# Kernel tuning notes

Measured on AMD Instinct MI355X. Metric: run time of the kernel, lower is better.

## Reference

```python
import jax, jax.numpy as jnp
import numpy as np
from jax import lax

EPS = 1e-5  # BatchNorm / LayerNorm eps
B, DIM, H, W = 32, 256, 64, 64
S = 64            # state_dim
D_INNER = 256     # ssd_expand * dim
HIDDEN = 1024     # mlp_ratio * dim


def _bn(x, g, b, m, v):
    # BatchNorm2d, inference mode with given running stats. x: (B,C,H,W)
    inv = lax.rsqrt(v + EPS)
    return (x - m[None, :, None, None]) * (g * inv)[None, :, None, None] + b[None, :, None, None]


def _dwconv3x3(x, w):
    # depthwise 3x3 conv, stride 1, SAME padding. w: (C,1,3,3)
    return lax.conv_general_dilated(
        x, w, window_strides=(1, 1), padding='SAME',
        feature_group_count=x.shape[1],
        dimension_numbers=('NCHW', 'OIHW', 'NCHW'))


def setup_inputs() -> dict:
    key = jax.random.key(0)
    ks = jax.random.split(key, 32)
    n = lambda i, shp, s=0.02: jax.random.normal(ks[i], shp, jnp.float32) * s
    u = lambda i, shp: jax.random.uniform(ks[i], shp, jnp.float32)
    return {
        'x': jax.random.normal(ks[0], (B, DIM, H, W), jnp.float32),
        # dwconv1 (Conv2dNorm depthwise)
        'dw1_w': n(1, (DIM, 1, 3, 3)), 'dw1_g': 1.0 + n(2, (DIM,)), 'dw1_b': n(3, (DIM,)),
        'dw1_m': n(4, (DIM,)), 'dw1_v': u(5, (DIM,)) + 0.5,
        # LayerNorm1d
        'ln_w': 1.0 + n(6, (DIM,)), 'ln_b': n(7, (DIM,)),
        # mixer (HSMSSD)
        'bcdt_w': n(8, (3 * S, DIM)),
        'dwm_w': n(9, (3 * S, 1, 3, 3)),
        'A_param': 1.0 + 15.0 * u(10, (S,)),
        'hz_w': n(11, (2 * D_INNER, DIM)),
        'out_w': n(12, (DIM, D_INNER)),
        'D_param': jnp.ones((1,), jnp.float32),
        # dwconv2
        'dw2_w': n(13, (DIM, 1, 3, 3)), 'dw2_g': 1.0 + n(14, (DIM,)), 'dw2_b': n(15, (DIM,)),
        'dw2_m': n(16, (DIM,)), 'dw2_v': u(17, (DIM,)) + 0.5,
        # FFN
        'fc1_w': n(18, (HIDDEN, DIM)), 'fc1_g': 1.0 + n(19, (HIDDEN,)), 'fc1_b': n(20, (HIDDEN,)),
        'fc1_m': n(21, (HIDDEN,)), 'fc1_v': u(22, (HIDDEN,)) + 0.5,
        'fc2_w': n(23, (DIM, HIDDEN)), 'fc2_g': 1.0 + n(24, (DIM,)), 'fc2_b': n(25, (DIM,)),
        'fc2_m': n(26, (DIM,)), 'fc2_v': u(27, (DIM,)) + 0.5,
        # alpha-gated residual blends
        'alpha': 1e-4 * jnp.ones((4, DIM), jnp.float32) + n(28, (4, DIM), 0.01),
    }


def reference(x, dw1_w, dw1_g, dw1_b, dw1_m, dw1_v, ln_w, ln_b,
              bcdt_w, dwm_w, A_param, hz_w, out_w, D_param,
              dw2_w, dw2_g, dw2_b, dw2_m, dw2_v,
              fc1_w, fc1_g, fc1_b, fc1_m, fc1_v,
              fc2_w, fc2_g, fc2_b, fc2_m, fc2_v, alpha):
    b, dim, h_, w_ = x.shape
    L = h_ * w_
    a = jax.nn.sigmoid(alpha)[:, :, None, None]  # (4, dim, 1, 1)

    # alpha-blended depthwise conv 1
    x = (1.0 - a[0]) * x + a[0] * _bn(_dwconv3x3(x, dw1_w), dw1_g, dw1_b, dw1_m, dw1_v)
    x_prev = x

    # LayerNorm1d over channel dim on (B, C, L)
    xf = x.reshape(b, dim, L)
    mean = xf.mean(axis=1, keepdims=True)
    var = ((xf - mean) ** 2).mean(axis=1, keepdims=True)
    xn = (xf - mean) * lax.rsqrt(var + EPS) * ln_w[None, :, None] + ln_b[None, :, None]

    # HSMSSD mixer
    bc_dt = jnp.einsum('bcl,oc->bol', xn, bcdt_w).reshape(b, 3 * S, h_, w_)
    bc_dt = _dwconv3x3(bc_dt, dwm_w).reshape(b, 3 * S, L)
    Bm, Cm, dt = jnp.split(bc_dt, 3, axis=1)          # each (B, S, L)
    Am = jax.nn.softmax(dt + A_param[None, :, None], axis=-1)
    AB = Am * Bm                                      # (B, S, L)
    h = jnp.einsum('bcl,bsl->bcs', xn, AB)            # (B, dim, S)
    hz = jnp.einsum('bcs,oc->bos', h, hz_w)           # (B, 2*d_inner, S)
    hh, z = jnp.split(hz, 2, axis=1)
    hg = hh * jax.nn.silu(z) + hh * D_param[0]
    hout = jnp.einsum('bcs,oc->bos', hg, out_w)       # (B, dim, S)
    y = jnp.einsum('bcs,bsl->bcl', hout, Cm).reshape(b, dim, h_, w_)

    x = (1.0 - a[1]) * x_prev + a[1] * y
    x = (1.0 - a[2]) * x + a[2] * _bn(_dwconv3x3(x, dw2_w), dw2_g, dw2_b, dw2_m, dw2_v)

    # FFN: 1x1 conv + BN + ReLU + 1x1 conv + BN
    t = _bn(jnp.einsum('bchw,oc->bohw', x, fc1_w), fc1_g, fc1_b, fc1_m, fc1_v)
    t = jax.nn.relu(t)
    t = _bn(jnp.einsum('bchw,oc->bohw', t, fc2_w), fc2_g, fc2_b, fc2_m, fc2_v)
    x = (1.0 - a[3]) * x + a[3] * t
    return (x, hout)
```

## Files before the change

### kernel.cpp

```cpp
#include <hip/hip_runtime.h>
#include <hip/hip_bf16.h>

typedef __hip_bfloat16 bf16;
typedef __attribute__((ext_vector_type(8))) short bf16x8;
typedef __attribute__((ext_vector_type(4))) float f32x4;

__device__ __forceinline__ float LD(const float* p){ return *p; }
__device__ __forceinline__ float LD(const bf16* p){ return __bfloat162float(*p); }
__device__ __forceinline__ void ST(float* p, float v){ *p = v; }
__device__ __forceinline__ void ST(bf16* p, float v){ *p = __float2bfloat16(v); }
__device__ __forceinline__ float sigm(float v){ return 1.f/(1.f + expf(-v)); }
__device__ __forceinline__ ushort f2b(float f){
    unsigned u = __float_as_uint(f);
    return (ushort)((u + 0x7fffu + ((u>>16)&1u)) >> 16);
}

#define NEPS 1e-5f

__global__ __launch_bounds__(256) void dwconv_bn_blend(
        const float* __restrict__ xin, float* __restrict__ xout,
        const float* __restrict__ w, const float* __restrict__ gg, const float* __restrict__ bb,
        const float* __restrict__ mm, const float* __restrict__ vv,
        const float* __restrict__ alpha, int arow)
{
    __shared__ float tile[66*66];
    int blk = blockIdx.x;
    int ch = blk & 255;
    const float* xp = xin + (size_t)blk*4096;
    float* op = xout + (size_t)blk*4096;
    int tid = threadIdx.x;
    for (int i = tid; i < 66*66; i += 256) {
        int r = i/66, c = i%66;
        int gr = r-1, gc = c-1;
        float val = 0.f;
        if (gr >= 0 && gr < 64 && gc >= 0 && gc < 64) val = xp[gr*64+gc];
        tile[i] = val;
    }
    __syncthreads();
    float wv[9];
    #pragma unroll
    for (int k=0;k<9;k++) wv[k] = w[ch*9+k];
    float sc = gg[ch] * rsqrtf(vv[ch] + NEPS);
    float mv = mm[ch], bv = bb[ch];
    float av = sigm(alpha[arow*256+ch]);
    for (int p = tid; p < 4096; p += 256) {
        int r = p>>6, c = p&63;
        float a = 0.f;
        #pragma unroll
        for (int dr=0;dr<3;dr++)
            #pragma unroll
            for (int dc=0;dc<3;dc++)
                a += wv[dr*3+dc]*tile[(r+dr)*66 + (c+dc)];
        float bn = (a - mv)*sc + bv;
        float xv = tile[(r+1)*66 + (c+1)];
        op[p] = (1.f-av)*xv + av*bn;
    }
}

__global__ __launch_bounds__(256) void ln_stats(const float* __restrict__ x1,
        float* __restrict__ meanp, float* __restrict__ invp)
{
    int blk = blockIdx.x;
    int b = blk >> 4;
    int l = ((blk & 15) << 8) + threadIdx.x;
    const float* xp = x1 + (size_t)b*256*4096 + l;
    float mean = 0.f, m2 = 0.f;
    for (int c=0;c<256;c++){ float v = xp[(size_t)c*4096]; mean += v; m2 += v*v; }
    mean *= (1.f/256.f); m2 *= (1.f/256.f);
    meanp[b*4096 + l] = mean;
    invp[b*4096 + l] = rsqrtf(m2 - mean*mean + NEPS);
}

__global__ __launch_bounds__(256) void prep_k(
        const float* __restrict__ f1w, const float* __restrict__ f2w,
        const float* __restrict__ bcdtw,
        const float* __restrict__ g1, const float* __restrict__ b1,
        const float* __restrict__ m1, const float* __restrict__ v1,
        const float* __restrict__ g2, const float* __restrict__ b2,
        const float* __restrict__ m2, const float* __restrict__ v2,
        ushort* __restrict__ w1bf, ushort* __restrict__ w2bf,
        ushort* __restrict__ wbc,
        float* __restrict__ sc1, float* __restrict__ sb1,
        float* __restrict__ sc2, float* __restrict__ sb2)
{
    int i = blockIdx.x*256 + threadIdx.x;
    if (i < 262144) {
        w1bf[i] = f2b(f1w[i]);
        w2bf[i] = f2b(f2w[i]);
    }
    if (i < 49152) wbc[i] = f2b(bcdtw[i]);
    if (i < 1024) { float s = g1[i]*rsqrtf(v1[i]+NEPS); sc1[i]=s; sb1[i]=b1[i]-m1[i]*s; }
    if (i < 256)  { float s = g2[i]*rsqrtf(v2[i]+NEPS); sc2[i]=s; sb2[i]=b2[i]-m2[i]*s; }
}

__global__ __launch_bounds__(256) void bcdt_mfma(
        const float* __restrict__ x1,
        const float* __restrict__ meanp, const float* __restrict__ invp,
        const float* __restrict__ lnw, const float* __restrict__ lnb,
        const ushort* __restrict__ wbc,
        bf16* __restrict__ bc, ushort* __restrict__ xn_bf, int b0)
{
    __shared__ __align__(16) ushort Xs[64*256];
    int blk = blockIdx.x;
    int lb = blk >> 6;
    int b  = b0 + lb;
    int l0 = (blk & 63) << 6;
    int tid = threadIdx.x, lane = tid & 63, w = tid >> 6;
    const float* xp = x1 + (size_t)b*256*4096 + l0;
    float mval = meanp[b*4096 + l0 + lane];
    float ival = invp [b*4096 + l0 + lane];
    ushort* xnp = xn_bf + (size_t)lb*256*4096 + l0;

    for (int cc = w*8; cc < 256; cc += 32) {
        ushort u[8];
        #pragma unroll
        for (int j=0;j<8;j++){
            float v = xp[(size_t)(cc+j)*4096 + lane];
            float xn = (v - mval)*ival*lnw[cc+j] + lnb[cc+j];
            u[j] = f2b(xn);
            xnp[(size_t)(cc+j)*4096 + lane] = u[j];
        }
        uint4 pk;
        pk.x = (uint)u[0] | ((uint)u[1]<<16);
        pk.y = (uint)u[2] | ((uint)u[3]<<16);
        pk.z = (uint)u[4] | ((uint)u[5]<<16);
        pk.w = (uint)u[6] | ((uint)u[7]<<16);
        int g = (cc>>3) ^ (lane&7);
        *(uint4*)&Xs[lane*256 + g*8] = pk;
    }
    __syncthreads();

    f32x4 zero4 = {0.f,0.f,0.f,0.f};
    f32x4 acc[3][4];
    #pragma unroll
    for (int m=0;m<3;m++)
        #pragma unroll
        for (int f=0;f<4;f++) acc[m][f] = zero4;

    int hbase = w*48;
    #pragma unroll
    for (int ks=0; ks<8; ks++){
        bf16x8 afr[3];
        #pragma unroll
        for (int m=0;m<3;m++)
            afr[m] = *(const bf16x8*)&wbc[(size_t)(hbase + m*16 + (lane&15))*256
                                          + ks*32 + (lane>>4)*8];
        #pragma unroll
        for (int f=0;f<4;f++){
            int px = f*16 + (lane&15);
            int g = (ks*4 + (lane>>4)) ^ (px&7);
            bf16x8 bfr = *(const bf16x8*)&Xs[px*256 + g*8];
            #pragma unroll
            for (int m=0;m<3;m++)
                acc[m][f] = __builtin_amdgcn_mfma_f32_16x16x32_bf16(afr[m], bfr, acc[m][f], 0,0,0);
        }
    }
    bf16* op = bc + (size_t)lb*192*4096 + l0;
    #pragma unroll
    for (int m=0;m<3;m++)
        #pragma unroll
        for (int r=0;r<4;r++){
            int o = hbase + m*16 + (lane>>4)*4 + r;
            #pragma unroll
            for (int f=0;f<4;f++){
                int px = f*16 + (lane&15);
                op[(size_t)o*4096 + px] = __float2bfloat16(acc[m][f][r]);
            }
        }
}

__global__ __launch_bounds__(256) void dwconv_plain(bf16* __restrict__ data, const float* __restrict__ w)
{
    __shared__ float tile[66*66];
    int blk = blockIdx.x;
    int ch = blk % 192;
    bf16* xp = data + (size_t)blk*4096;
    int tid = threadIdx.x;
    for (int i = tid; i < 66*66; i += 256) {
        int r = i/66, c = i%66;
        int gr = r-1, gc = c-1;
        float val = 0.f;
        if (gr >= 0 && gr < 64 && gc >= 0 && gc < 64) val = LD(&xp[gr*64+gc]);
        tile[i] = val;
    }
    __syncthreads();
    float wv[9];
    #pragma unroll
    for (int k=0;k<9;k++) wv[k] = w[ch*9+k];
    for (int p = tid; p < 4096; p += 256) {
        int r = p>>6, c = p&63;
        float a = 0.f;
        #pragma unroll
        for (int dr=0;dr<3;dr++)
            #pragma unroll
            for (int dc=0;dc<3;dc++)
                a += wv[dr*3+dc]*tile[(r+dr)*66 + (c+dc)];
        ST(&xp[p], a);
    }
}

__global__ __launch_bounds__(256) void softmax_ab(bf16* __restrict__ bc, const float* __restrict__ A)
{
    __shared__ float red[8];
    int blk = blockIdx.x;
    int lb = blk >> 6;
    int s = blk & 63;
    bf16* dtp = bc + ((size_t)lb*192 + 128 + s)*4096;
    bf16* bmp = bc + ((size_t)lb*192 + s)*4096;
    int tid = threadIdx.x;
    float Av = A[s];
    float vals[16];
    float mx = -1e30f;
    #pragma unroll
    for (int i=0;i<16;i++){ vals[i] = LD(&dtp[i*256+tid]) + Av; mx = fmaxf(mx, vals[i]); }
    #pragma unroll
    for (int o=32;o>0;o>>=1) mx = fmaxf(mx, __shfl_down(mx, o));
    int lane = tid & 63, wid = tid >> 6;
    if (lane == 0) red[wid] = mx;
    __syncthreads();
    if (tid == 0) red[4] = fmaxf(fmaxf(red[0],red[1]), fmaxf(red[2],red[3]));
    __syncthreads();
    mx = red[4];
    float sum = 0.f;
    #pragma unroll
    for (int i=0;i<16;i++){ vals[i] = expf(vals[i]-mx); sum += vals[i]; }
    #pragma unroll
    for (int o=32;o>0;o>>=1) sum += __shfl_down(sum, o);
    if (lane == 0) red[wid] = sum;
    __syncthreads();
    if (tid == 0) red[5] = red[0]+red[1]+red[2]+red[3];
    __syncthreads();
    float inv = 1.f/red[5];
    #pragma unroll
    for (int i=0;i<16;i++){
        float ab = vals[i]*inv*LD(&bmp[i*256+tid]);
        ST(&bmp[i*256+tid], ab);
    }
}

__global__ __launch_bounds__(256) void h_mfma(
        const ushort* __restrict__ xn_bf, const bf16* __restrict__ bc,
        float* __restrict__ h_part)
{
    int blk = blockIdx.x;
    int lb = blk >> 3;
    int kz = blk & 7;
    int kbase = kz*512;
    int tid = threadIdx.x, lane = tid & 63, w = tid >> 6;
    const ushort* ap = xn_bf + (size_t)lb*256*4096;
    const ushort* bp = (const ushort*)bc + (size_t)lb*192*4096;
    f32x4 zero4 = {0.f,0.f,0.f,0.f};
    f32x4 acc[4][4];
    #pragma unroll
    for (int m=0;m<4;m++)
        #pragma unroll
        for (int n=0;n<4;n++) acc[m][n] = zero4;

    for (int ks=0; ks<16; ks++){
        int koff = kbase + ks*32 + (lane>>4)*8;
        bf16x8 afr[4], bfr[4];
        #pragma unroll
        for (int m=0;m<4;m++)
            afr[m] = *(const bf16x8*)&ap[(size_t)(w*64 + m*16 + (lane&15))*4096 + koff];
        #pragma unroll
        for (int n=0;n<4;n++)
            bfr[n] = *(const bf16x8*)&bp[(size_t)(n*16 + (lane&15))*4096 + koff];
        #pragma unroll
        for (int m=0;m<4;m++)
            #pragma unroll
            for (int n=0;n<4;n++)
                acc[m][n] = __builtin_amdgcn_mfma_f32_16x16x32_bf16(afr[m], bfr[n], acc[m][n], 0,0,0);
    }
    float* hp = h_part + ((size_t)lb*8 + kz)*16384;
    #pragma unroll
    for (int m=0;m<4;m++)
        #pragma unroll
        for (int n=0;n<4;n++)
            #pragma unroll
            for (int r=0;r<4;r++){
                int c = w*64 + m*16 + (lane>>4)*4 + r;
                int s = n*16 + (lane&15);
                hp[c*64 + s] = acc[m][n][r];
            }
}

__global__ __launch_bounds__(256) void hz_gemm(const float* __restrict__ h_part,
        const float* __restrict__ w, float* __restrict__ hz)
{
    __shared__ float ht[256][64];
    int blk = blockIdx.x; int lb = blk>>3; int o0 = (blk&7)*64;
    int tid = threadIdx.x;
    const float* hp = h_part + (size_t)lb*8*16384;
    for (int i=tid;i<16384;i+=256){
        float s = 0.f;
        #pragma unroll
        for (int k=0;k<8;k++) s += hp[k*16384 + i];
        ht[i>>6][i&63] = s;
    }
    __syncthreads();
    int lane=tid&63, g=tid>>6;
    for (int i4=0;i4<4;i4++){
        int ol = g*16 + i4*4;
        const float* r0 = w + (size_t)(o0+ol)*256;
        const float *r1=r0+256, *r2=r0+512, *r3=r0+768;
        float d0=0.f,d1=0.f,d2=0.f,d3=0.f;
        #pragma unroll 8
        for (int c4=0;c4<64;c4++){
            float x0=ht[c4*4][lane],x1v=ht[c4*4+1][lane],x2v=ht[c4*4+2][lane],x3v=ht[c4*4+3][lane];
            float4 a0=((const float4*)r0)[c4],a1=((const float4*)r1)[c4];
            float4 a2=((const float4*)r2)[c4],a3=((const float4*)r3)[c4];
            d0 += a0.x*x0+a0.y*x1v+a0.z*x2v+a0.w*x3v;
            d1 += a1.x*x0+a1.y*x1v+a1.z*x2v+a1.w*x3v;
            d2 += a2.x*x0+a2.y*x1v+a2.z*x2v+a2.w*x3v;
            d3 += a3.x*x0+a3.y*x1v+a3.z*x2v+a3.w*x3v;
        }
        size_t base = ((size_t)lb*512 + o0 + ol)*64 + lane;
        hz[base]=d0; hz[base+64]=d1; hz[base+128]=d2; hz[base+192]=d3;
    }
}

__global__ void gate_k(const float* __restrict__ hz, float* __restrict__ hg, const float* __restrict__ Dp)
{
    int i = blockIdx.x*256 + threadIdx.x;
    int lb = i >> 14;
    int r = i & 16383;
    const float* hp = hz + (size_t)lb*32768;
    float hh = hp[r], z = hp[16384 + r];
    float sil = z / (1.f + expf(-z));
    hg[i] = hh * (sil + Dp[0]);
}

__global__ __launch_bounds__(256) void out_gemm(const float* __restrict__ hg, const float* __restrict__ w,
        ushort* __restrict__ hout_bf, float* __restrict__ hout_out, int b0)
{
    __shared__ float ht[256][64];
    int blk = blockIdx.x; int lb = blk>>2; int b = b0 + lb; int o0 = (blk&3)*64;
    int tid = threadIdx.x;
    const float* hp = hg + (size_t)lb*16384;
    for (int i=tid;i<16384;i+=256) ht[i>>6][i&63]=hp[i];
    __syncthreads();
    int lane=tid&63, g=tid>>6;
    for (int i4=0;i4<4;i4++){
        int ol = g*16 + i4*4;
        const float* r0 = w + (size_t)(o0+ol)*256;
        const float *r1=r0+256, *r2=r0+512, *r3=r0+768;
        float d0=0.f,d1=0.f,d2=0.f,d3=0.f;
        #pragma unroll 8
        for (int c4=0;c4<64;c4++){
            float x0=ht[c4*4][lane],x1v=ht[c4*4+1][lane],x2v=ht[c4*4+2][lane],x3v=ht[c4*4+3][lane];
            float4 a0=((const float4*)r0)[c4],a1=((const float4*)r1)[c4];
            float4 a2=((const float4*)r2)[c4],a3=((const float4*)r3)[c4];
            d0 += a0.x*x0+a0.y*x1v+a0.z*x2v+a0.w*x3v;
            d1 += a1.x*x0+a1.y*x1v+a1.z*x2v+a1.w*x3v;
            d2 += a2.x*x0+a2.y*x1v+a2.z*x2v+a2.w*x3v;
            d3 += a3.x*x0+a3.y*x1v+a3.z*x2v+a3.w*x3v;
        }
        size_t lbase = ((size_t)lb*256 + o0 + ol)*64 + lane;
        hout_bf[lbase]=f2b(d0); hout_bf[lbase+64]=f2b(d1);
        hout_bf[lbase+128]=f2b(d2); hout_bf[lbase+192]=f2b(d3);
        size_t gbase = ((size_t)b*256 + o0 + ol)*64 + lane;
        hout_out[gbase]=d0; hout_out[gbase+64]=d1;
        hout_out[gbase+128]=d2; hout_out[gbase+192]=d3;
    }
}

__global__ __launch_bounds__(256) void y_mfma(
        const ushort* __restrict__ hout_bf, const bf16* __restrict__ bc,
        float* __restrict__ x1, const float* __restrict__ alpha, int b0)
{
    __shared__ __align__(16) ushort Cs[64*64];
    int blk = blockIdx.x; int lb = blk>>6; int b = b0 + lb; int l0 = (blk&63)<<6;
    int tid = threadIdx.x, lane = tid&63, w = tid>>6;
    const ushort* cp = (const ushort*)bc + ((size_t)lb*192 + 64)*4096 + l0;
    for (int sc = w*8; sc < 64; sc += 32){
        ushort u[8];
        #pragma unroll
        for (int j=0;j<8;j++) u[j] = cp[(size_t)(sc+j)*4096 + lane];
        uint4 pk;
        pk.x = (uint)u[0] | ((uint)u[1]<<16);
        pk.y = (uint)u[2] | ((uint)u[3]<<16);
        pk.z = (uint)u[4] | ((uint)u[5]<<16);
        pk.w = (uint)u[6] | ((uint)u[7]<<16);
        int g = (sc>>3) ^ (lane&7);
        *(uint4*)&Cs[lane*64 + g*8] = pk;
    }
    __syncthreads();

    f32x4 zero4 = {0.f,0.f,0.f,0.f};
    f32x4 acc[4][4];
    #pragma unroll
    for (int m=0;m<4;m++)
        #pragma unroll
        for (int f=0;f<4;f++) acc[m][f] = zero4;

    const ushort* ap = hout_bf + (size_t)lb*256*64;
    #pragma unroll
    for (int ks=0; ks<2; ks++){
        bf16x8 afr[4];
        #pragma unroll
        for (int m=0;m<4;m++)
            afr[m] = *(const bf16x8*)&ap[(size_t)(w*64 + m*16 + (lane&15))*64
                                          + ks*32 + (lane>>4)*8];
        #pragma unroll
        for (int f=0;f<4;f++){
            int px = f*16 + (lane&15);
            int s8 = ks*32 + (lane>>4)*8;
            int g = (s8>>3) ^ (px&7);
            bf16x8 bfr = *(const bf16x8*)&Cs[px*64 + g*8];
            #pragma unroll
            for (int m=0;m<4;m++)
                acc[m][f] = __builtin_amdgcn_mfma_f32_16x16x32_bf16(afr[m], bfr, acc[m][f], 0,0,0);
        }
    }

    float* xpo = x1 + (size_t)b*256*4096 + l0;
    #pragma unroll
    for (int m=0;m<4;m++)
        #pragma unroll
        for (int r=0;r<4;r++){
            int c = w*64 + m*16 + (lane>>4)*4 + r;
            float av = sigm(alpha[256+c]);
            #pragma unroll
            for (int f=0;f<4;f++){
                int px = f*16 + (lane&15);
                float xv = xpo[(size_t)c*4096 + px];
                xpo[(size_t)c*4096 + px] = (1.f-av)*xv + av*acc[m][f][r];
            }
        }
}

__global__ __launch_bounds__(256) void transpose_k(const float* __restrict__ x1,
        ushort* __restrict__ xT)
{
    __shared__ ushort T[64*258];
    int blk = blockIdx.x;
    int b = blk >> 6, l0 = (blk & 63) << 6;
    int tid = threadIdx.x;
    const float* xp = x1 + (size_t)b*256*4096 + l0;
    for (int i = tid; i < 16384; i += 256){
        int c = i >> 6, l = i & 63;
        T[l*258 + c] = f2b(xp[(size_t)c*4096 + l]);
    }
    __syncthreads();
    int l = tid & 63, cseg = (tid >> 6) << 6;
    ushort* op = xT + ((size_t)b*4096 + l0 + l)*256 + cseg;
    const ushort* tp = &T[l*258 + cseg];
    #pragma unroll
    for (int j=0;j<8;j++){
        uint4 v;
        v.x = (uint)tp[j*8+0] | ((uint)tp[j*8+1]<<16);
        v.y = (uint)tp[j*8+2] | ((uint)tp[j*8+3]<<16);
        v.z = (uint)tp[j*8+4] | ((uint)tp[j*8+5]<<16);
        v.w = (uint)tp[j*8+6] | ((uint)tp[j*8+7]<<16);
        *(uint4*)&op[j*8] = v;
    }
}

__global__ __launch_bounds__(256) void ffn_mfma_t(
        const ushort* __restrict__ xT,
        const float* __restrict__ x,
        const ushort* __restrict__ w1bf,
        const ushort* __restrict__ w2bf,
        const float* __restrict__ sc1, const float* __restrict__ sb1,
        const float* __restrict__ sc2, const float* __restrict__ sb2,
        const float* __restrict__ alpha,
        float* __restrict__ out)
{
    __shared__ __align__(16) ushort Ts[64*128];
    int blk = blockIdx.x;
    int b = blk >> 6, l0 = (blk & 63) << 6;
    int tid = threadIdx.x, lane = tid & 63, w = tid >> 6;
    const ushort* xtp = xT + ((size_t)b*4096 + l0)*256;
    const float* xp = x + (size_t)b*256*4096 + l0;

    f32x4 zero4 = {0.f,0.f,0.f,0.f};
    f32x4 acc2[4][4];
    #pragma unroll
    for (int m=0;m<4;m++)
        #pragma unroll
        for (int f=0;f<4;f++) acc2[m][f] = zero4;

    for (int hc = 0; hc < 1024; hc += 128) {
        int hbase = hc + w*32;
        f32x4 c1[2][4];
        #pragma unroll
        for (int m=0;m<2;m++)
            #pragma unroll
            for (int f=0;f<4;f++) c1[m][f] = zero4;
        for (int ks = 0; ks < 8; ks++) {
            bf16x8 afr[2];
            #pragma unroll
            for (int m=0;m<2;m++)
                afr[m] = *(const bf16x8*)&w1bf[(size_t)(hbase + m*16 + (lane&15))*256
                                               + ks*32 + (lane>>4)*8];
            #pragma unroll
            for (int f=0;f<4;f++){
                bf16x8 bfr = *(const bf16x8*)&xtp[(size_t)(f*16 + (lane&15))*256
                                                  + ks*32 + (lane>>4)*8];
                #pragma unroll
                for (int m=0;m<2;m++)
                    c1[m][f] = __builtin_amdgcn_mfma_f32_16x16x32_bf16(afr[m], bfr, c1[m][f], 0,0,0);
            }
        }
        __syncthreads();
        #pragma unroll
        for (int m=0;m<2;m++){
            int hl0 = w*32 + m*16 + ((lane>>4)<<2);
            int h0 = hc + hl0;
            float s0=sc1[h0], s1=sc1[h0+1], s2=sc1[h0+2], s3=sc1[h0+3];
            float q0=sb1[h0], q1=sb1[h0+1], q2=sb1[h0+2], q3=sb1[h0+3];
            int gbase = hl0>>3;
            #pragma unroll
            for (int f=0;f<4;f++){
                int px = f*16 + (lane&15);
                float t0 = fmaxf(c1[m][f][0]*s0 + q0, 0.f);
                float t1 = fmaxf(c1[m][f][1]*s1 + q1, 0.f);
                float t2 = fmaxf(c1[m][f][2]*s2 + q2, 0.f);
                float t3 = fmaxf(c1[m][f][3]*s3 + q3, 0.f);
                uint2 pk;
                pk.x = (uint)f2b(t0) | ((uint)f2b(t1)<<16);
                pk.y = (uint)f2b(t2) | ((uint)f2b(t3)<<16);
                int g = gbase ^ (px&7);
                *(uint2*)&Ts[px*128 + g*8 + (hl0&7)] = pk;
            }
        }
        __syncthreads();
        int c0 = w*64;
        for (int ks = 0; ks < 4; ks++) {
            bf16x8 afr[4];
            #pragma unroll
            for (int m=0;m<4;m++)
                afr[m] = *(const bf16x8*)&w2bf[(size_t)(c0 + m*16 + (lane&15))*1024
                                               + hc + ks*32 + (lane>>4)*8];
            #pragma unroll
            for (int f=0;f<4;f++){
                int px = f*16 + (lane&15);
                int hl = ks*32 + (lane>>4)*8;
                int g = (hl>>3) ^ (px&7);
                bf16x8 bfr = *(const bf16x8*)&Ts[px*128 + g*8];
                #pragma unroll
                for (int m=0;m<4;m++)
                    acc2[m][f] = __builtin_amdgcn_mfma_f32_16x16x32_bf16(afr[m], bfr, acc2[m][f], 0,0,0);
            }
        }
    }

    float* op = out + (size_t)b*256*4096 + l0;
    int c0 = w*64;
    #pragma unroll
    for (int m=0;m<4;m++){
        #pragma unroll
        for (int r=0;r<4;r++){
            int c = c0 + m*16 + (lane>>4)*4 + r;
            float a = sigm(alpha[768+c]);
            float s2 = sc2[c], bb2 = sb2[c];
            #pragma unroll
            for (int f=0;f<4;f++){
                int px = f*16 + (lane&15);
                float t2 = acc2[m][f][r]*s2 + bb2;
                float xv = xp[(size_t)c*4096 + px];
                op[(size_t)c*4096 + px] = (1.f-a)*xv + a*t2;
            }
        }
    }
}

__global__ __launch_bounds__(256) void ffn_mfma(
        const float* __restrict__ x,
        const ushort* __restrict__ w1bf, const ushort* __restrict__ w2bf,
        const float* __restrict__ sc1, const float* __restrict__ sb1,
        const float* __restrict__ sc2, const float* __restrict__ sb2,
        const float* __restrict__ alpha, float* __restrict__ out)
{
    __shared__ __align__(16) ushort Xs[64*256];
    __shared__ __align__(16) ushort Ts[64*128];
    int blk = blockIdx.x;
    int b = blk >> 6, l0 = (blk & 63) << 6;
    int tid = threadIdx.x, lane = tid & 63, w = tid >> 6;
    const float* xp = x + (size_t)b*256*4096 + l0;

    for (int cc = w*8; cc < 256; cc += 32) {
        float v[8];
        #pragma unroll
        for (int j=0;j<8;j++) v[j] = xp[(size_t)(cc+j)*4096 + lane];
        uint4 pk;
        pk.x = (uint)f2b(v[0]) | ((uint)f2b(v[1])<<16);
        pk.y = (uint)f2b(v[2]) | ((uint)f2b(v[3])<<16);
        pk.z = (uint)f2b(v[4]) | ((uint)f2b(v[5])<<16);
        pk.w = (uint)f2b(v[6]) | ((uint)f2b(v[7])<<16);
        int g = (cc>>3) ^ (lane&7);
        *(uint4*)&Xs[lane*256 + g*8] = pk;
    }
    __syncthreads();

    f32x4 zero4 = {0.f,0.f,0.f,0.f};
    f32x4 acc2[4][4];
    #pragma unroll
    for (int m=0;m<4;m++)
        #pragma unroll
        for (int f=0;f<4;f++) acc2[m][f] = zero4;

    for (int hc = 0; hc < 1024; hc += 128) {
        int hbase = hc + w*32;
        f32x4 c1[2][4];
        #pragma unroll
        for (int m=0;m<2;m++)
            #pragma unroll
            for (int f=0;f<4;f++) c1[m][f] = zero4;
        for (int ks = 0; ks < 8; ks++) {
            bf16x8 afr[2];
            #pragma unroll
            for (int m=0;m<2;m++)
                afr[m] = *(const bf16x8*)&w1bf[(size_t)(hbase + m*16 + (lane&15))*256
                                               + ks*32 + (lane>>4)*8];
            #pragma unroll
            for (int f=0;f<4;f++){
                int px = f*16 + (lane&15);
                int g = (ks*4 + (lane>>4)) ^ (px&7);
                bf16x8 bfr = *(const bf16x8*)&Xs[px*256 + g*8];
                #pragma unroll
                for (int m=0;m<2;m++)
                    c1[m][f] = __builtin_amdgcn_mfma_f32_16x16x32_bf16(afr[m], bfr, c1[m][f], 0,0,0);
            }
        }
        __syncthreads();
        #pragma unroll
        for (int m=0;m<2;m++){
            int hl0 = w*32 + m*16 + ((lane>>4)<<2);
            int h0 = hc + hl0;
            float s0=sc1[h0], s1=sc1[h0+1], s2=sc1[h0+2], s3=sc1[h0+3];
            float q0=sb1[h0], q1=sb1[h0+1], q2=sb1[h0+2], q3=sb1[h0+3];
            int gbase = hl0>>3;
            #pragma unroll
            for (int f=0;f<4;f++){
                int px = f*16 + (lane&15);
                float t0 = fmaxf(c1[m][f][0]*s0 + q0, 0.f);
                float t1 = fmaxf(c1[m][f][1]*s1 + q1, 0.f);
                float t2 = fmaxf(c1[m][f][2]*s2 + q2, 0.f);
                float t3 = fmaxf(c1[m][f][3]*s3 + q3, 0.f);
                uint2 pk;
                pk.x = (uint)f2b(t0) | ((uint)f2b(t1)<<16);
                pk.y = (uint)f2b(t2) | ((uint)f2b(t3)<<16);
                int g = gbase ^ (px&7);
                *(uint2*)&Ts[px*128 + g*8 + (hl0&7)] = pk;
            }
        }
        __syncthreads();
        int c0 = w*64;
        for (int ks = 0; ks < 4; ks++) {
            bf16x8 afr[4];
            #pragma unroll
            for (int m=0;m<4;m++)
                afr[m] = *(const bf16x8*)&w2bf[(size_t)(c0 + m*16 + (lane&15))*1024
                                               + hc + ks*32 + (lane>>4)*8];
            #pragma unroll
            for (int f=0;f<4;f++){
                int px = f*16 + (lane&15);
                int hl = ks*32 + (lane>>4)*8;
                int g = (hl>>3) ^ (px&7);
                bf16x8 bfr = *(const bf16x8*)&Ts[px*128 + g*8];
                #pragma unroll
                for (int m=0;m<4;m++)
                    acc2[m][f] = __builtin_amdgcn_mfma_f32_16x16x32_bf16(afr[m], bfr, acc2[m][f], 0,0,0);
            }
        }
    }

    float* op = out + (size_t)b*256*4096 + l0;
    int c0 = w*64;
    #pragma unroll
    for (int m=0;m<4;m++){
        #pragma unroll
        for (int r=0;r<4;r++){
            int c = c0 + m*16 + (lane>>4)*4 + r;
            float a = sigm(alpha[768+c]);
            float s2 = sc2[c], bb2 = sb2[c];
            #pragma unroll
            for (int f=0;f<4;f++){
                int px = f*16 + (lane&15);
                float t2 = acc2[m][f][r]*s2 + bb2;
                float xv = xp[(size_t)c*4096 + px];
                op[(size_t)c*4096 + px] = (1.f-a)*xv + a*t2;
            }
        }
    }
}

extern "C" void kernel_launch(void* const* d_in, const int* in_sizes, int n_in,
                              void* d_out, int out_size, void* d_ws, size_t ws_size,
                              hipStream_t stream)
{
    (void)in_sizes; (void)n_in; (void)out_size;
    const float* x     = (const float*)d_in[0];
    const float* dw1w  = (const float*)d_in[1];
    const float* dw1g  = (const float*)d_in[2];
    const float* dw1b  = (const float*)d_in[3];
    const float* dw1m  = (const float*)d_in[4];
    const float* dw1v  = (const float*)d_in[5];
    const float* lnw   = (const float*)d_in[6];
    const float* lnb   = (const float*)d_in[7];
    const float* bcdtw = (const float*)d_in[8];
    const float* dwmw  = (const float*)d_in[9];
    const float* Ap    = (const float*)d_in[10];
    const float* hzw   = (const float*)d_in[11];
    const float* outw  = (const float*)d_in[12];
    const float* Dp    = (const float*)d_in[13];
    const float* dw2w  = (const float*)d_in[14];
    const float* dw2g  = (const float*)d_in[15];
    const float* dw2b  = (const float*)d_in[16];
    const float* dw2m  = (const float*)d_in[17];
    const float* dw2v  = (const float*)d_in[18];
    const float* f1w   = (const float*)d_in[19];
    const float* f1g   = (const float*)d_in[20];
    const float* f1b   = (const float*)d_in[21];
    const float* f1m   = (const float*)d_in[22];
    const float* f1v   = (const float*)d_in[23];
    const float* f2w   = (const float*)d_in[24];
    const float* f2g   = (const float*)d_in[25];
    const float* f2b_  = (const float*)d_in[26];
    const float* f2m   = (const float*)d_in[27];
    const float* f2v   = (const float*)d_in[28];
    const float* alpha = (const float*)d_in[29];

    const size_t nx = (size_t)32*256*4096;
    float* x1 = (float*)d_out;
    float* hout_out = x1 + nx;

    char* ws = (char*)d_ws;
    float* meanp = (float*)ws;
    float* invp  = meanp + 131072;
    size_t off = 1048576;
    ushort* w1bf = (ushort*)(ws + off); off += 524288;
    ushort* w2bf = (ushort*)(ws + off); off += 524288;
    ushort* wbc  = (ushort*)(ws + off); off += 98304;
    float* sc1 = (float*)(ws + off); off += 4096;
    float* sb1 = (float*)(ws + off); off += 4096;
    float* sc2 = (float*)(ws + off); off += 1024;
    float* sb2 = (float*)(ws + off); off += 1024;
    off = (off + 255) & ~(size_t)255;

    const size_t xt_bytes = nx*2;
    ushort* xT = nullptr;
    size_t rem = ws_size > off ? ws_size - off : 0;
    const size_t perb = 1572864 + 2097152 + 524288 + 131072 + 65536 + 32768;
    if (rem >= xt_bytes + perb) { xT = (ushort*)(ws + off); off += xt_bytes; }
    char* cbase = ws + off;
    size_t avail = ws_size > off ? ws_size - off : 0;

    int NB = 1;
    for (int nb = 32; nb >= 1; nb >>= 1) if (avail >= (size_t)nb*perb) { NB = nb; break; }

    prep_k<<<1024,256,0,stream>>>(f1w, f2w, bcdtw, f1g,f1b,f1m,f1v, f2g,f2b_,f2m,f2v,
                                  w1bf, w2bf, wbc, sc1, sb1, sc2, sb2);
    dwconv_bn_blend<<<8192,256,0,stream>>>(x, x1, dw1w,dw1g,dw1b,dw1m,dw1v, alpha, 0);
    ln_stats<<<512,256,0,stream>>>(x1, meanp, invp);

    bf16*   bc      = (bf16*)cbase;
    ushort* xn_bf   = (ushort*)(cbase + (size_t)NB*1572864);
    float*  h_part  = (float*)(cbase + (size_t)NB*(1572864 + 2097152));
    float*  hz      = (float*)((char*)h_part + (size_t)NB*524288);
    float*  hg      = (float*)((char*)hz + (size_t)NB*131072);
    ushort* hout_bf = (ushort*)((char*)hg + (size_t)NB*65536);

    for (int b0 = 0; b0 < 32; b0 += NB) {
        bcdt_mfma<<<NB*64,256,0,stream>>>(x1, meanp, invp, lnw, lnb, wbc, bc, xn_bf, b0);
        dwconv_plain<<<NB*192,256,0,stream>>>(bc, dwmw);
        softmax_ab<<<NB*64,256,0,stream>>>(bc, Ap);
        h_mfma<<<NB*8,256,0,stream>>>(xn_bf, bc, h_part);
        hz_gemm<<<NB*8,256,0,stream>>>(h_part, hzw, hz);
        gate_k<<<NB*64,256,0,stream>>>(hz, hg, Dp);
        out_gemm<<<NB*4,256,0,stream>>>(hg, outw, hout_bf, hout_out, b0);
        y_mfma<<<NB*64,256,0,stream>>>(hout_bf, bc, x1, alpha, b0);
    }

    dwconv_bn_blend<<<8192,256,0,stream>>>(x1, x1, dw2w,dw2g,dw2b,dw2m,dw2v, alpha, 2);
    if (xT) {
        transpose_k<<<2048,256,0,stream>>>(x1, xT);
        ffn_mfma_t<<<2048,256,0,stream>>>(xT, x1, w1bf, w2bf, sc1, sb1, sc2, sb2, alpha, x1);
    } else {
        ffn_mfma<<<2048,256,0,stream>>>(x1, w1bf, w2bf, sc1, sb1, sc2, sb2, alpha, x1);
    }
}
```

Baseline: 828.8 us.

## Restructure FFN kernel: per-wave pixel rows, LDS-staged weights via direct global-to-LDS loads

Reworks the fused FFN kernel so each wave owns 16 pixels, keeps its transposed activation fragments in registers for the whole hidden loop, and stages 64-row chunks of fc1 and fc2 weights into swizzled shared memory with global_load_lds. The intermediate ReLU tile becomes per-wave, so block-wide barriers are only needed around the weight staging. This is meant to cut repeated global weight reads across waves and reduce synchronisation. In exchange it uses more LDS and registers (16 accumulator tiles plus 8 fragments), which may lower occupancy, and weight loads are not double-buffered.

```diff
diff --git a/kernel.cpp b/kernel.cpp
--- a/kernel.cpp
+++ b/kernel.cpp
@@ -13,6 +13,10 @@
 __device__ __forceinline__ ushort f2b(float f){
     unsigned u = __float_as_uint(f);
     return (ushort)((u + 0x7fffu + ((u>>16)&1u)) >> 16);
+}
+__device__ __forceinline__ void gload_lds16(const ushort* g, ushort* l){
+    __builtin_amdgcn_global_load_lds((const __attribute__((address_space(1))) unsigned int*)g,
+                                     (__attribute__((address_space(3))) unsigned int*)l, 16, 0, 0);
 }
 
 #define NEPS 1e-5f
@@ -456,7 +460,7 @@
     }
 }
 
-__global__ __launch_bounds__(256) void ffn_mfma_t(
+__global__ __launch_bounds__(256) void ffn_mfma_t2(
         const ushort* __restrict__ xT,
         const float* __restrict__ x,
         const ushort* __restrict__ w1bf,
@@ -466,101 +470,103 @@
         const float* __restrict__ alpha,
         float* __restrict__ out)
 {
-    __shared__ __align__(16) ushort Ts[64*128];
+    __shared__ __align__(16) ushort W1s[64*256];
+    __shared__ __align__(16) ushort W2s[256*64];
+    __shared__ __align__(16) ushort Ts[4*16*64];
     int blk = blockIdx.x;
     int b = blk >> 6, l0 = (blk & 63) << 6;
     int tid = threadIdx.x, lane = tid & 63, w = tid >> 6;
-    const ushort* xtp = xT + ((size_t)b*4096 + l0)*256;
+    int q = lane >> 4, lp = lane & 15;
+    int px = w*16 + lp;
+
+    const ushort* xtp = xT + ((size_t)b*4096 + l0 + px)*256;
+    bf16x8 xfrag[8];
+    #pragma unroll
+    for (int ks=0; ks<8; ks++)
+        xfrag[ks] = *(const bf16x8*)&xtp[ks*32 + q*8];
+
+    f32x4 zero4 = {0.f,0.f,0.f,0.f};
+    f32x4 acc2[16];
+    #pragma unroll
+    for (int m=0;m<16;m++) acc2[m] = zero4;
+
+    ushort* tsw = &Ts[w*1024];
+
+    for (int hc = 0; hc < 16; ++hc) {
+        if (hc) __syncthreads();
+        #pragma unroll
+        for (int it=0; it<8; ++it) {
+            int s = it*256 + w*64 + lane;
+            {
+                int h = s >> 5, j = s & 31;
+                const ushort* src = w1bf + (size_t)(hc*64 + h)*256 + ((j ^ (h&7))<<3);
+                gload_lds16(src, &W1s[(size_t)(it*256 + w*64)*8]);
+            }
+            {
+                int c = s >> 3, j = s & 7;
+                const ushort* src = w2bf + (size_t)c*1024 + hc*64 + ((j ^ (c&7))<<3);
+                gload_lds16(src, &W2s[(size_t)(it*256 + w*64)*8]);
+            }
+        }
+        __syncthreads();
+
+        f32x4 c1[4];
+        #pragma unroll
+        for (int m=0;m<4;m++) c1[m] = zero4;
+        #pragma unroll
+        for (int ks=0; ks<8; ks++){
+            bf16x8 bfr = xfrag[ks];
+            #pragma unroll
+            for (int m=0;m<4;m++){
+                int row = m*16 + lp;
+                int j = ks*4 + q;
+                bf16x8 afr = *(const bf16x8*)&W1s[row*256 + ((j ^ (row&7))<<3)];
+                c1[m] = __builtin_amdgcn_mfma_f32_16x16x32_bf16(afr, bfr, c1[m], 0,0,0);
+            }
+        }
+
+        #pragma unroll
+        for (int m=0;m<4;m++){
+            int hl = m*16 + q*4;
+            int hg = hc*64 + hl;
+            float s0=sc1[hg],s1=sc1[hg+1],s2v=sc1[hg+2],s3=sc1[hg+3];
+            float q0=sb1[hg],q1=sb1[hg+1],q2v=sb1[hg+2],q3=sb1[hg+3];
+            float t0 = fmaxf(c1[m][0]*s0 + q0, 0.f);
+            float t1 = fmaxf(c1[m][1]*s1 + q1, 0.f);
+            float t2 = fmaxf(c1[m][2]*s2v + q2v, 0.f);
+            float t3 = fmaxf(c1[m][3]*s3 + q3, 0.f);
+            uint2 pk;
+            pk.x = (uint)f2b(t0) | ((uint)f2b(t1)<<16);
+            pk.y = (uint)f2b(t2) | ((uint)f2b(t3)<<16);
+            int u = m*4 + q;
+            int slot = u >> 1, rem = (u & 1) << 3;
+            *(uint2*)((char*)&tsw[lp*64] + (((slot ^ (lp&7))<<4) + rem)) = pk;
+        }
+
+        #pragma unroll
+        for (int ks2=0; ks2<2; ks2++){
+            int sr = ks2*4 + q;
+            bf16x8 bfr = *(const bf16x8*)((const char*)&tsw[lp*64] + ((sr ^ (lp&7))<<4));
+            #pragma unroll
+            for (int m=0;m<16;m++){
+                int c = m*16 + lp;
+                bf16x8 afr = *(const bf16x8*)&W2s[c*64 + ((sr ^ (c&7))<<3)];
+                acc2[m] = __builtin_amdgcn_mfma_f32_16x16x32_bf16(afr, bfr, acc2[m], 0,0,0);
+            }
+        }
+    }
+
     const float* xp = x + (size_t)b*256*4096 + l0;
-
-    f32x4 zero4 = {0.f,0.f,0.f,0.f};
-    f32x4 acc2[4][4];
-    #pragma unroll
-    for (int m=0;m<4;m++)
-        #pragma unroll
-        for (int f=0;f<4;f++) acc2[m][f] = zero4;
-
-    for (int hc = 0; hc < 1024; hc += 128) {
-        int hbase = hc + w*32;
-        f32x4 c1[2][4];
-        #pragma unroll
-        for (int m=0;m<2;m++)
-            #pragma unroll
-            for (int f=0;f<4;f++) c1[m][f] = zero4;
-        for (int ks = 0; ks < 8; ks++) {
-            bf16x8 afr[2];
-            #pragma unroll
-            for (int m=0;m<2;m++)
-                afr[m] = *(const bf16x8*)&w1bf[(size_t)(hbase + m*16 + (lane&15))*256
-                                               + ks*32 + (lane>>4)*8];
-            #pragma unroll
-            for (int f=0;f<4;f++){
-                bf16x8 bfr = *(const bf16x8*)&xtp[(size_t)(f*16 + (lane&15))*256
-                                                  + ks*32 + (lane>>4)*8];
-                #pragma unroll
-                for (int m=0;m<2;m++)
-                    c1[m][f] = __builtin_amdgcn_mfma_f32_16x16x32_bf16(afr[m], bfr, c1[m][f], 0,0,0);
-            }
-        }
-        __syncthreads();
-        #pragma unroll
-        for (int m=0;m<2;m++){
-            int hl0 = w*32 + m*16 + ((lane>>4)<<2);
-            int h0 = hc + hl0;
-            float s0=sc1[h0], s1=sc1[h0+1], s2=sc1[h0+2], s3=sc1[h0+3];
-            float q0=sb1[h0], q1=sb1[h0+1], q2=sb1[h0+2], q3=sb1[h0+3];
-            int gbase = hl0>>3;
-            #pragma unroll
-            for (int f=0;f<4;f++){
-                int px = f*16 + (lane&15);
-                float t0 = fmaxf(c1[m][f][0]*s0 + q0, 0.f);
-                float t1 = fmaxf(c1[m][f][1]*s1 + q1, 0.f);
-                float t2 = fmaxf(c1[m][f][2]*s2 + q2, 0.f);
-                float t3 = fmaxf(c1[m][f][3]*s3 + q3, 0.f);
-                uint2 pk;
-                pk.x = (uint)f2b(t0) | ((uint)f2b(t1)<<16);
-                pk.y = (uint)f2b(t2) | ((uint)f2b(t3)<<16);
-                int g = gbase ^ (px&7);
-                *(uint2*)&Ts[px*128 + g*8 + (hl0&7)] = pk;
-            }
-        }
-        __syncthreads();
-        int c0 = w*64;
-        for (int ks = 0; ks < 4; ks++) {
-            bf16x8 afr[4];
-            #pragma unroll
-            for (int m=0;m<4;m++)
-                afr[m] = *(const bf16x8*)&w2bf[(size_t)(c0 + m*16 + (lane&15))*1024
-                                               + hc + ks*32 + (lane>>4)*8];
-            #pragma unroll
-            for (int f=0;f<4;f++){
-                int px = f*16 + (lane&15);
-                int hl = ks*32 + (lane>>4)*8;
-                int g = (hl>>3) ^ (px&7);
-                bf16x8 bfr = *(const bf16x8*)&Ts[px*128 + g*8];
-                #pragma unroll
-                for (int m=0;m<4;m++)
-                    acc2[m][f] = __builtin_amdgcn_mfma_f32_16x16x32_bf16(afr[m], bfr, acc2[m][f], 0,0,0);
-            }
-        }
-    }
-
     float* op = out + (size_t)b*256*4096 + l0;
-    int c0 = w*64;
-    #pragma unroll
-    for (int m=0;m<4;m++){
+    #pragma unroll
+    for (int m=0;m<16;m++){
         #pragma unroll
         for (int r=0;r<4;r++){
-            int c = c0 + m*16 + (lane>>4)*4 + r;
+            int c = m*16 + q*4 + r;
             float a = sigm(alpha[768+c]);
-            float s2 = sc2[c], bb2 = sb2[c];
-            #pragma unroll
-            for (int f=0;f<4;f++){
-                int px = f*16 + (lane&15);
-                float t2 = acc2[m][f][r]*s2 + bb2;
-                float xv = xp[(size_t)c*4096 + px];
-                op[(size_t)c*4096 + px] = (1.f-a)*xv + a*t2;
-            }
+            float t2 = acc2[m][r]*sc2[c] + sb2[c];
+            float xv = xp[(size_t)c*4096 + px];
+            op[(size_t)c*4096 + px] = (1.f-a)*xv + a*t2;
         }
     }
 }
@@ -776,7 +782,7 @@
     dwconv_bn_blend<<<8192,256,0,stream>>>(x1, x1, dw2w,dw2g,dw2b,dw2m,dw2v, alpha, 2);
     if (xT) {
         transpose_k<<<2048,256,0,stream>>>(x1, xT);
-        ffn_mfma_t<<<2048,256,0,stream>>>(xT, x1, w1bf, w2bf, sc1, sb1, sc2, sb2, alpha, x1);
+        ffn_mfma_t2<<<2048,256,0,stream>>>(xT, x1, w1bf, w2bf, sc1, sb1, sc2, sb2, alpha, x1);
     } else {
         ffn_mfma<<<2048,256,0,stream>>>(x1, w1bf, w2bf, sc1, sb1, sc2, sb2, alpha, x1);
     }
```

After: 829.6 us. Within noise of the previous version (+0.1%).
